# Performance work log

Measured on AMD Instinct MI355X. Metric: run time of the kernel, lower is better.

## Reference

```python
import jax, jax.numpy as jnp
import numpy as np

N_NODES = 50000
N_EDGES = 800000
HIDDEN = 128
N_GRAPHS = 128


def setup_inputs() -> dict:
    key = jax.random.key(0)
    ks = jax.random.split(key, 12)
    x = jax.random.normal(ks[0], (N_NODES, HIDDEN), dtype=jnp.float32)
    edge_index = jax.random.randint(ks[1], (2, N_EDGES), 0, N_NODES, dtype=jnp.int64)
    batch = jnp.sort(jax.random.randint(ks[2], (N_NODES,), 0, N_GRAPHS, dtype=jnp.int64))
    s = 1.0 / np.sqrt(HIDDEN)
    def lin(k):
        return jax.random.uniform(k, (HIDDEN, HIDDEN), jnp.float32, -s, s)
    return {
        "x": x,
        "edge_index": edge_index,
        "batch": batch,
        # layer 1 SAGEConv: lin_l (neighbor, with bias), lin_r (root, no bias)
        "wl1": lin(ks[3]), "b1": jax.random.uniform(ks[4], (HIDDEN,), jnp.float32, -s, s), "wr1": lin(ks[5]),
        # layer 2 SAGEConv
        "wl2": lin(ks[6]), "b2": jax.random.uniform(ks[7], (HIDDEN,), jnp.float32, -s, s), "wr2": lin(ks[8]),
        # classifier Linear
        "cw": lin(ks[9]), "cb": jax.random.uniform(ks[10], (HIDDEN,), jnp.float32, -s, s),
    }


def _sage_conv(x, src, dst, wl, b, wr, n_nodes):
    # mean aggregation of source features onto destination nodes
    agg = jax.ops.segment_sum(x[src], dst, num_segments=n_nodes)      # [N, H]
    deg = jax.ops.segment_sum(jnp.ones_like(dst, x.dtype), dst, num_segments=n_nodes)
    mean = agg / jnp.maximum(deg, 1.0)[:, None]
    # out = lin_l(mean) + lin_r(x); lin_l carries the bias (PyG convention)
    return mean @ wl.T + b + x @ wr.T


def reference(x, edge_index, batch, wl1, b1, wr1, wl2, b2, wr2, cw, cb):
    src, dst = edge_index[0], edge_index[1]
    n = x.shape[0]
    h = jax.nn.relu(_sage_conv(x, src, dst, wl1, b1, wr1, n))
    h = jax.nn.relu(_sage_conv(h, src, dst, wl2, b2, wr2, n))
    # global mean pool over graphs (dropout p=0.0 -> identity)
    gsum = jax.ops.segment_sum(h, batch, num_segments=N_GRAPHS)       # [G, H]
    gcnt = jax.ops.segment_sum(jnp.ones((n,), h.dtype), batch, num_segments=N_GRAPHS)
    pooled = gsum / jnp.maximum(gcnt, 1.0)[:, None]
    return pooled @ cw.T + cb
```

## Files before the change

### kernel.cpp

```cpp
#include <hip/hip_runtime.h>
#include <cstdint>
#include <cstddef>

#define HID 128
#define LDK 72
#define EPB 4096
#define CAP 8192

typedef __attribute__((ext_vector_type(8))) short short8;
typedef __attribute__((ext_vector_type(4))) float floatx4;

#if __has_builtin(__builtin_amdgcn_cvt_pk_f32_fp8) && __has_builtin(__builtin_amdgcn_cvt_pk_fp8_f32)
#define HW_FP8 1
#else
#define HW_FP8 0
#endif

__device__ __forceinline__ unsigned short f2bf(float f) {
  union { float f; uint32_t u; } c; c.f = f;
  uint32_t u = c.u;
  uint32_t r = (u + 0x7FFFu + ((u >> 16) & 1u)) >> 16;
  return (unsigned short)r;
}
__device__ __forceinline__ float bflo(uint32_t v) { return __uint_as_float(v << 16); }
__device__ __forceinline__ float bfhi(uint32_t v) { return __uint_as_float(v & 0xFFFF0000u); }
__device__ __forceinline__ float bf2f(unsigned short s) { return __uint_as_float(((uint32_t)s) << 16); }

__device__ __forceinline__ uint32_t f2fp8_sw(float v) {
  uint32_t u = __float_as_uint(v);
  uint32_t s = (u >> 24) & 0x80u;
  uint32_t af = u & 0x7FFFFFFFu;
  if (__uint_as_float(af) < 0.015625f) return s;
  uint32_t r = af + 0x7FFFFu + ((af >> 20) & 1u);
  return s | ((r >> 20) - 960u);
}
__device__ __forceinline__ float fp8dec_sw(uint32_t b) {
  uint32_t mag = b & 0x7Fu;
  uint32_t v = ((b & 0x80u) << 24) | ((mag << 20) + 0x3C000000u);
  return mag ? __uint_as_float(v) : 0.0f;
}

__device__ __forceinline__ uint32_t pack_fp8x4(float a, float b, float c, float d) {
#if HW_FP8
  int p = __builtin_amdgcn_cvt_pk_fp8_f32(a, b, 0, false);
  p = __builtin_amdgcn_cvt_pk_fp8_f32(c, d, p, true);
  return (uint32_t)p;
#else
  return f2fp8_sw(a) | (f2fp8_sw(b) << 8) | (f2fp8_sw(c) << 16) | (f2fp8_sw(d) << 24);
#endif
}

__device__ __forceinline__ void acc_fp8x4(float* __restrict__ a, uint32_t w) {
#if HW_FP8
  auto lo = __builtin_amdgcn_cvt_pk_f32_fp8(w, false);
  auto hi = __builtin_amdgcn_cvt_pk_f32_fp8(w, true);
  a[0] += lo[0]; a[1] += lo[1]; a[2] += hi[0]; a[3] += hi[1];
#else
  a[0] += fp8dec_sw(w & 255);
  a[1] += fp8dec_sw((w >> 8) & 255);
  a[2] += fp8dec_sw((w >> 16) & 255);
  a[3] += fp8dec_sw(w >> 24);
#endif
}


__global__ __launch_bounds__(256) void k_bucket(const int* __restrict__ src,
                                                const int* __restrict__ dst,
                                                int* __restrict__ bcur,
                                                uint32_t* __restrict__ ebuf,
                                                int E, int NB) {
  __shared__ int hist[256];
  __shared__ int lcur[256];
  const int t = threadIdx.x;
  const int base = blockIdx.x * EPB;
  hist[t] = 0;
  __syncthreads();

  uint32_t val[EPB / 256];
  int bk[EPB / 256];
  #pragma unroll
  for (int i = 0; i < EPB / 256; ++i) {
    int e = base + i * 256 + t;
    bk[i] = -1;
    if (e < E) {
      int d = dst[e];
      int s = src[e];
      bk[i] = d >> 8;
      val[i] = (uint32_t)s | ((uint32_t)(d & 255) << 16);
      atomicAdd(&hist[bk[i]], 1);
    }
  }
  __syncthreads();
  if (t < NB) {
    int c = hist[t];
    lcur[t] = c ? atomicAdd(&bcur[t], c) : 0;
  }
  __syncthreads();
  #pragma unroll
  for (int i = 0; i < EPB / 256; ++i) {
    if (bk[i] >= 0) {
      int pos = bk[i] * CAP + atomicAdd(&lcur[bk[i]], 1);
      ebuf[pos] = val[i];
    }
  }
}

__global__ __launch_bounds__(256) void k_bucket_fill2(const uint32_t* __restrict__ ebuf,
                                                      const int* __restrict__ bcur,
                                                      int* __restrict__ rowbeg,
                                                      int* __restrict__ rowend,
                                                      unsigned short* __restrict__ csr16,
                                                      int N) {
  __shared__ int hist[256];
  __shared__ int scan[256];
  const int b = blockIdx.x;
  const int t = threadIdx.x;
  hist[t] = 0;
  __syncthreads();
  const int lo = b * CAP;
  const int hi = lo + bcur[b];
  for (int i = lo + t; i < hi; i += 256) atomicAdd(&hist[ebuf[i] >> 16], 1);
  __syncthreads();
  int v = hist[t];
  scan[t] = v;
  __syncthreads();
  #pragma unroll
  for (int off = 1; off < 256; off <<= 1) {
    int add = (t >= off) ? scan[t - off] : 0;
    __syncthreads();
    scan[t] += add;
    __syncthreads();
  }
  int excl = scan[t] - v;
  int node = (b << 8) + t;
  if (node < N) {
    rowbeg[node] = lo + excl;
    rowend[node] = lo + excl + v;
  }
  hist[t] = lo + excl;
  __syncthreads();
  for (int i = lo + t; i < hi; i += 256) {
    uint32_t e = ebuf[i];
    int pos = atomicAdd(&hist[e >> 16], 1);
    csr16[pos] = (unsigned short)(e & 0xFFFFu);
  }
}


__global__ __launch_bounds__(256) void k_cast_dual(const float* __restrict__ src,
                                                   unsigned short* __restrict__ dst,
                                                   uint32_t* __restrict__ q, int n4) {
  int i = blockIdx.x * 256 + threadIdx.x;
  if (i < n4) {
    float4 v = ((const float4*)src)[i];
    uint32_t lo = (uint32_t)f2bf(v.x) | ((uint32_t)f2bf(v.y) << 16);
    uint32_t hi = (uint32_t)f2bf(v.z) | ((uint32_t)f2bf(v.w) << 16);
    ((uint2*)dst)[i] = make_uint2(lo, hi);
    q[i] = pack_fp8x4(v.x, v.y, v.z, v.w);
  }
}


__global__ __launch_bounds__(256) void k_cast_bf2q(const unsigned short* __restrict__ src,
                                                   uint32_t* __restrict__ q, int n4) {
  int i = blockIdx.x * 256 + threadIdx.x;
  if (i < n4) {
    uint2 v = ((const uint2*)src)[i];
    q[i] = pack_fp8x4(bflo(v.x), bfhi(v.x), bflo(v.y), bfhi(v.y));
  }
}


__global__ __launch_bounds__(256) void k_aggregate(const unsigned char* __restrict__ featq,
                                                   const int* __restrict__ rowbeg,
                                                   const int* __restrict__ rowend,
                                                   const unsigned short* __restrict__ csr16,
                                                   unsigned short* __restrict__ outmean, int N) {
  int wid = blockIdx.x * 4 + (threadIdx.x >> 6);
  int lane = threadIdx.x & 63;
  if (wid >= N) return;
  int start = rowbeg[wid];
  int end   = rowend[wid];
  const int grp = lane >> 4;
  const int fl  = lane & 15;
  float a[8];
  #pragma unroll
  for (int i = 0; i < 8; ++i) a[i] = 0.f;

  for (int base = start; base < end; base += 64) {
    int m = end - base;
    if (m > 64) m = 64;
    int sidx = (base + lane < end) ? (int)csr16[base + lane] : 0;
    for (int j = 0; j < m; j += 16) {
      int j0 = j + grp, j1 = j + grp + 4, j2 = j + grp + 8, j3 = j + grp + 12;
      int s0 = __shfl(sidx, j0, 64);
      int s1 = __shfl(sidx, j1, 64);
      int s2 = __shfl(sidx, j2, 64);
      int s3 = __shfl(sidx, j3, 64);
      bool g0 = j0 < m, g1 = j1 < m, g2 = j2 < m, g3 = j3 < m;
      uint2 v0, v1, v2, v3;
      if (g0) v0 = *(const uint2*)(featq + (size_t)s0 * HID + fl * 8);
      if (g1) v1 = *(const uint2*)(featq + (size_t)s1 * HID + fl * 8);
      if (g2) v2 = *(const uint2*)(featq + (size_t)s2 * HID + fl * 8);
      if (g3) v3 = *(const uint2*)(featq + (size_t)s3 * HID + fl * 8);
      if (g0) { acc_fp8x4(a, v0.x); acc_fp8x4(a + 4, v0.y); }
      if (g1) { acc_fp8x4(a, v1.x); acc_fp8x4(a + 4, v1.y); }
      if (g2) { acc_fp8x4(a, v2.x); acc_fp8x4(a + 4, v2.y); }
      if (g3) { acc_fp8x4(a, v3.x); acc_fp8x4(a + 4, v3.y); }
    }
  }
  #pragma unroll
  for (int i = 0; i < 8; ++i) {
    a[i] += __shfl_xor(a[i], 16, 64);
    a[i] += __shfl_xor(a[i], 32, 64);
  }
  if (grp == 0) {
    int deg = end - start;
    float inv = 1.0f / (float)(deg > 1 ? deg : 1);
    uint4 o;
    o.x = (uint32_t)f2bf(a[0] * inv) | ((uint32_t)f2bf(a[1] * inv) << 16);
    o.y = (uint32_t)f2bf(a[2] * inv) | ((uint32_t)f2bf(a[3] * inv) << 16);
    o.z = (uint32_t)f2bf(a[4] * inv) | ((uint32_t)f2bf(a[5] * inv) << 16);
    o.w = (uint32_t)f2bf(a[6] * inv) | ((uint32_t)f2bf(a[7] * inv) << 16);
    *(uint4*)(outmean + (size_t)wid * HID + fl * 8) = o;
  }
}


__global__ __launch_bounds__(256, 2) void k_gemm_mfma(const unsigned short* __restrict__ A1,
                                                      const unsigned short* __restrict__ A2,
                                                      const float* __restrict__ WL,
                                                      const float* __restrict__ WR,
                                                      const float* __restrict__ bias,
                                                      unsigned short* __restrict__ outb,
                                                      const int* __restrict__ batch,
                                                      float* __restrict__ pooled,
                                                      int M, int relu) {
  __shared__ __align__(16) unsigned short sAB[2 * 128 * LDK];
  __shared__ int sB[128];
  unsigned short* sA = sAB;
  unsigned short* sW = sAB + 128 * LDK;
  const int t = threadIdx.x;
  const int lane = t & 63;
  const int wave = t >> 6;
  const int row0 = blockIdx.x * 128;
  const int mhalf = (wave & 1) * 64;
  const int nhalf = (wave >> 1) * 64;
  const int ml = lane & 15;
  const int q  = lane >> 4;

  floatx4 acc[4][4];
  #pragma unroll
  for (int a = 0; a < 4; ++a)
    #pragma unroll
    for (int b = 0; b < 4; ++b) acc[a][b] = (floatx4){0.f, 0.f, 0.f, 0.f};

  for (int stage = 0; stage < 4; ++stage) {
    const unsigned short* __restrict__ Asrc = (stage < 2) ? A1 : A2;
    const float* __restrict__ Wsrc = (stage < 2) ? WL : WR;
    const int k0g = (stage & 1) * 64;
    if (stage) __syncthreads();

    #pragma unroll
    for (int i = 0; i < 4; ++i) {
      int seg = t + i * 256;
      int r = seg >> 3, kc = (seg & 7) * 8;
      int gr = row0 + r;
      float4 v = make_float4(0.f, 0.f, 0.f, 0.f);
      if (gr < M) v = *(const float4*)(Asrc + (size_t)gr * HID + k0g + kc);
      *(float4*)&sA[r * LDK + kc] = v;
    }
    #pragma unroll
    for (int i = 0; i < 8; ++i) {
      int e = t + i * 256;
      int o = e >> 4, kc = (e & 15) * 4;
      float4 v = *(const float4*)(Wsrc + (size_t)o * HID + k0g + kc);
      uint32_t lo = (uint32_t)f2bf(v.x) | ((uint32_t)f2bf(v.y) << 16);
      uint32_t hi = (uint32_t)f2bf(v.z) | ((uint32_t)f2bf(v.w) << 16);
      *(uint2*)&sW[o * LDK + kc] = make_uint2(lo, hi);
    }
    __syncthreads();

    #pragma unroll
    for (int ks = 0; ks < 2; ++ks) {
      int kb = ks * 32 + q * 8;
      short8 af[4], bfr[4];
      #pragma unroll
      for (int mt = 0; mt < 4; ++mt)
        af[mt] = *(const short8*)&sA[(mhalf + mt * 16 + ml) * LDK + kb];
      #pragma unroll
      for (int nt = 0; nt < 4; ++nt)
        bfr[nt] = *(const short8*)&sW[(nhalf + nt * 16 + ml) * LDK + kb];
      #pragma unroll
      for (int mt = 0; mt < 4; ++mt)
        #pragma unroll
        for (int nt = 0; nt < 4; ++nt)
          acc[mt][nt] = __builtin_amdgcn_mfma_f32_16x16x32_bf16(af[mt], bfr[nt], acc[mt][nt], 0, 0, 0);
    }
  }

  if (pooled == nullptr) {
    #pragma unroll
    for (int nt = 0; nt < 4; ++nt) {
      int gcol = nhalf + nt * 16 + ml;
      float bv = bias[gcol];
      #pragma unroll
      for (int mt = 0; mt < 4; ++mt) {
        #pragma unroll
        for (int r = 0; r < 4; ++r) {
          int grow = row0 + mhalf + mt * 16 + q * 4 + r;
          if (grow < M) {
            float v = acc[mt][nt][r] + bv;
            if (relu) v = fmaxf(v, 0.f);
            outb[(size_t)grow * HID + gcol] = f2bf(v);
          }
        }
      }
    }
  } else {
    __syncthreads();
    unsigned short* sH = sAB;
    #pragma unroll
    for (int nt = 0; nt < 4; ++nt) {
      int gcol = nhalf + nt * 16 + ml;
      float bv = bias[gcol];
      #pragma unroll
      for (int mt = 0; mt < 4; ++mt) {
        #pragma unroll
        for (int r = 0; r < 4; ++r) {
          int lr = mhalf + mt * 16 + q * 4 + r;
          float v = acc[mt][nt][r] + bv;
          if (relu) v = fmaxf(v, 0.f);
          sH[lr * 128 + gcol] = f2bf(v);
        }
      }
    }
    if (t < 128) sB[t] = (row0 + t < M) ? batch[row0 + t] : -1;
    __syncthreads();
    const int f = t & 127, half = t >> 7;
    float pacc = 0.f;
    int curg = -1;
    for (int n = half; n < 128; n += 2) {
      int g = sB[n];
      if (g != curg) {
        if (curg >= 0) atomicAdd(&pooled[(size_t)curg * HID + f], pacc);
        curg = g; pacc = 0.f;
      }
      if (g >= 0) pacc += bf2f(sH[n * 128 + f]);
    }
    if (curg >= 0) atomicAdd(&pooled[(size_t)curg * HID + f], pacc);
  }
}


__device__ __forceinline__ int lower_bound_dev(const int* a, int n, int key) {
  int lo = 0, hi = n;
  while (lo < hi) {
    int mid = (lo + hi) >> 1;
    if (a[mid] < key) lo = mid + 1; else hi = mid;
  }
  return lo;
}

__global__ __launch_bounds__(256) void k_classify(const float* __restrict__ pooled,
                                                  const int* __restrict__ batch,
                                                  const float* __restrict__ cw,
                                                  const float* __restrict__ cb,
                                                  float* __restrict__ out, int N) {
  __shared__ int bnds[2];
  __shared__ float sp[128];
  __shared__ float part[2][128];
  int g = blockIdx.x;
  int t = threadIdx.x;
  if (t == 0) bnds[0] = lower_bound_dev(batch, N, g);
  if (t == 1) bnds[1] = lower_bound_dev(batch, N, g + 1);
  __syncthreads();
  int cnt = bnds[1] - bnds[0];
  float inv = 1.0f / (float)(cnt > 1 ? cnt : 1);
  if (t < 128) sp[t] = pooled[(size_t)g * HID + t] * inv;
  __syncthreads();
  int o = t & 127, kh = t >> 7;
  float a = 0.f;
  #pragma unroll 4
  for (int k = kh * 64; k < kh * 64 + 64; ++k) a += sp[k] * cw[(size_t)o * HID + k];
  part[kh][o] = a;
  __syncthreads();
  if (t < 128) out[(size_t)g * HID + t] = part[0][t] + part[1][t] + cb[t];
}


extern "C" void kernel_launch(void* const* d_in, const int* in_sizes, int n_in,
                              void* d_out, int out_size, void* d_ws, size_t ws_size,
                              hipStream_t stream) {
  const float* x     = (const float*)d_in[0];
  const int*   ei    = (const int*)d_in[1];
  const int*   batch = (const int*)d_in[2];
  const float* wl1   = (const float*)d_in[3];
  const float* b1    = (const float*)d_in[4];
  const float* wr1   = (const float*)d_in[5];
  const float* wl2   = (const float*)d_in[6];
  const float* b2    = (const float*)d_in[7];
  const float* wr2   = (const float*)d_in[8];
  const float* cw    = (const float*)d_in[9];
  const float* cb    = (const float*)d_in[10];
  float* out = (float*)d_out;

  const int N = in_sizes[0] / HID;
  const int E = in_sizes[1] / 2;
  const int G = out_size / HID;
  const int* src = ei;
  const int* dst = ei + E;

  char* w = (char*)d_ws;
  int*      bcur   = (int*)(w);
  float*    pooled = (float*)(w + 1024);
  int*      rowbeg = (int*)(w + 66560);
  int*      rowend = (int*)(w + 266560);
  uint32_t* ebuf   = (uint32_t*)(w + 466944);
  unsigned short* csr16 = (unsigned short*)(w + 6889472);
  unsigned short* xb    = (unsigned short*)(w + 10100736);
  unsigned short* meanb = (unsigned short*)(w + 10100736 + 12800000);
  unsigned short* h1b   = (unsigned short*)(w + 10100736 + 25600000);
  unsigned char*  xq    = (unsigned char*)(w + 10100736 + 38400000);
  unsigned char*  h1q   = (unsigned char*)(w + 10100736 + 44800000);

  const int NB = (N + 255) >> 8;
  const int aggBlocks  = (N + 3) / 4;
  const int gemmBlocks = (N + 127) / 128;
  const int castBlocks = (N * HID / 4 + 255) / 256;
  const int bktBlocks  = (E + EPB - 1) / EPB;

  hipMemsetAsync(w, 0, 66560, stream);

  hipLaunchKernelGGL(k_bucket,       dim3(bktBlocks), dim3(256), 0, stream, src, dst, bcur, ebuf, E, NB);
  hipLaunchKernelGGL(k_bucket_fill2, dim3(NB),  dim3(256), 0, stream, ebuf, bcur, rowbeg, rowend, csr16, N);
  hipLaunchKernelGGL(k_cast_dual,    dim3(castBlocks), dim3(256), 0, stream, x, xb, (uint32_t*)xq, N * HID / 4);

  hipLaunchKernelGGL(k_aggregate, dim3(aggBlocks), dim3(256), 0, stream, xq, rowbeg, rowend, csr16, meanb, N);
  hipLaunchKernelGGL(k_gemm_mfma, dim3(gemmBlocks), dim3(256), 0, stream, meanb, xb, wl1, wr1, b1, h1b,
                     (const int*)nullptr, (float*)nullptr, N, 1);
  hipLaunchKernelGGL(k_cast_bf2q, dim3(castBlocks), dim3(256), 0, stream, h1b, (uint32_t*)h1q, N * HID / 4);
  hipLaunchKernelGGL(k_aggregate, dim3(aggBlocks), dim3(256), 0, stream, h1q, rowbeg, rowend, csr16, meanb, N);
  hipLaunchKernelGGL(k_gemm_mfma, dim3(gemmBlocks), dim3(256), 0, stream, meanb, h1b, wl2, wr2, b2,
                     (unsigned short*)nullptr, batch, pooled, N, 1);
  hipLaunchKernelGGL(k_classify, dim3(G), dim3(256), 0, stream, pooled, batch, cw, cb, out, N);
}
```

Measured before the change: 229.7 us.

## Fuse fp8 quantization into GEMM epilogue and aggregate two nodes per wave

Removes the separate bf16-to-fp8 cast kernel by writing the fp8 copy of layer-1 output directly from the GEMM epilogue. This saves one launch and one full read and write pass over the hidden features. The aggregation kernel now processes two destination nodes per wavefront, interleaving their gathers to raise memory-level parallelism and halve the wave count. The risks are higher register pressure, imbalance when the two nodes have different degrees, and byte-granular scattered stores in the GEMM epilogue.

Measured after the change: 227.0 us. Within noise of the previous version (-1.2%).

```diff
diff --git a/kernel.cpp b/kernel.cpp
--- a/kernel.cpp
+++ b/kernel.cpp
@@ -47,6 +47,14 @@
   return (uint32_t)p;
 #else
   return f2fp8_sw(a) | (f2fp8_sw(b) << 8) | (f2fp8_sw(c) << 16) | (f2fp8_sw(d) << 24);
+#endif
+}
+
+__device__ __forceinline__ unsigned char f2fp8_one(float v) {
+#if HW_FP8
+  return (unsigned char)(__builtin_amdgcn_cvt_pk_fp8_f32(v, v, 0, false) & 0xFF);
+#else
+  return (unsigned char)f2fp8_sw(v);
 #endif
 }
 
@@ -161,68 +169,87 @@
 }
 
 
-__global__ __launch_bounds__(256) void k_cast_bf2q(const unsigned short* __restrict__ src,
-                                                   uint32_t* __restrict__ q, int n4) {
-  int i = blockIdx.x * 256 + threadIdx.x;
-  if (i < n4) {
-    uint2 v = ((const uint2*)src)[i];
-    q[i] = pack_fp8x4(bflo(v.x), bfhi(v.x), bflo(v.y), bfhi(v.y));
-  }
-}
-
-
 __global__ __launch_bounds__(256) void k_aggregate(const unsigned char* __restrict__ featq,
                                                    const int* __restrict__ rowbeg,
                                                    const int* __restrict__ rowend,
                                                    const unsigned short* __restrict__ csr16,
                                                    unsigned short* __restrict__ outmean, int N) {
-  int wid = blockIdx.x * 4 + (threadIdx.x >> 6);
+  int wpair = blockIdx.x * 4 + (threadIdx.x >> 6);
+  int n0 = wpair * 2;
+  int n1 = n0 + 1;
   int lane = threadIdx.x & 63;
-  if (wid >= N) return;
-  int start = rowbeg[wid];
-  int end   = rowend[wid];
+  if (n0 >= N) return;
   const int grp = lane >> 4;
   const int fl  = lane & 15;
-  float a[8];
-  #pragma unroll
-  for (int i = 0; i < 8; ++i) a[i] = 0.f;
-
-  for (int base = start; base < end; base += 64) {
-    int m = end - base;
-    if (m > 64) m = 64;
-    int sidx = (base + lane < end) ? (int)csr16[base + lane] : 0;
-    for (int j = 0; j < m; j += 16) {
+
+  int b0 = rowbeg[n0], e0 = rowend[n0];
+  int b1 = 0, e1 = 0;
+  if (n1 < N) { b1 = rowbeg[n1]; e1 = rowend[n1]; }
+  const int d0 = e0 - b0, d1 = e1 - b1;
+
+  float a0[8], a1[8];
+  #pragma unroll
+  for (int i = 0; i < 8; ++i) { a0[i] = 0.f; a1[i] = 0.f; }
+
+  while (b0 < e0 || b1 < e1) {
+    int m0 = e0 - b0; if (m0 < 0) m0 = 0; if (m0 > 64) m0 = 64;
+    int m1 = e1 - b1; if (m1 < 0) m1 = 0; if (m1 > 64) m1 = 64;
+    int sidx0 = (b0 + lane < e0) ? (int)csr16[b0 + lane] : 0;
+    int sidx1 = (b1 + lane < e1) ? (int)csr16[b1 + lane] : 0;
+    int mm = m0 > m1 ? m0 : m1;
+    for (int j = 0; j < mm; j += 16) {
       int j0 = j + grp, j1 = j + grp + 4, j2 = j + grp + 8, j3 = j + grp + 12;
-      int s0 = __shfl(sidx, j0, 64);
-      int s1 = __shfl(sidx, j1, 64);
-      int s2 = __shfl(sidx, j2, 64);
-      int s3 = __shfl(sidx, j3, 64);
-      bool g0 = j0 < m, g1 = j1 < m, g2 = j2 < m, g3 = j3 < m;
-      uint2 v0, v1, v2, v3;
-      if (g0) v0 = *(const uint2*)(featq + (size_t)s0 * HID + fl * 8);
-      if (g1) v1 = *(const uint2*)(featq + (size_t)s1 * HID + fl * 8);
-      if (g2) v2 = *(const uint2*)(featq + (size_t)s2 * HID + fl * 8);
-      if (g3) v3 = *(const uint2*)(featq + (size_t)s3 * HID + fl * 8);
-      if (g0) { acc_fp8x4(a, v0.x); acc_fp8x4(a + 4, v0.y); }
-      if (g1) { acc_fp8x4(a, v1.x); acc_fp8x4(a + 4, v1.y); }
-      if (g2) { acc_fp8x4(a, v2.x); acc_fp8x4(a + 4, v2.y); }
-      if (g3) { acc_fp8x4(a, v3.x); acc_fp8x4(a + 4, v3.y); }
-    }
-  }
+      int s00 = __shfl(sidx0, j0, 64), s01 = __shfl(sidx0, j1, 64);
+      int s02 = __shfl(sidx0, j2, 64), s03 = __shfl(sidx0, j3, 64);
+      int s10 = __shfl(sidx1, j0, 64), s11 = __shfl(sidx1, j1, 64);
+      int s12 = __shfl(sidx1, j2, 64), s13 = __shfl(sidx1, j3, 64);
+      bool p00 = j0 < m0, p01 = j1 < m0, p02 = j2 < m0, p03 = j3 < m0;
+      bool p10 = j0 < m1, p11 = j1 < m1, p12 = j2 < m1, p13 = j3 < m1;
+      uint2 u00, u01, u02, u03, u10, u11, u12, u13;
+      if (p00) u00 = *(const uint2*)(featq + (size_t)s00 * HID + fl * 8);
+      if (p01) u01 = *(const uint2*)(featq + (size_t)s01 * HID + fl * 8);
+      if (p02) u02 = *(const uint2*)(featq + (size_t)s02 * HID + fl * 8);
+      if (p03) u03 = *(const uint2*)(featq + (size_t)s03 * HID + fl * 8);
+      if (p10) u10 = *(const uint2*)(featq + (size_t)s10 * HID + fl * 8);
+      if (p11) u11 = *(const uint2*)(featq + (size_t)s11 * HID + fl * 8);
+      if (p12) u12 = *(const uint2*)(featq + (size_t)s12 * HID + fl * 8);
+      if (p13) u13 = *(const uint2*)(featq + (size_t)s13 * HID + fl * 8);
+      if (p00) { acc_fp8x4(a0, u00.x); acc_fp8x4(a0 + 4, u00.y); }
+      if (p01) { acc_fp8x4(a0, u01.x); acc_fp8x4(a0 + 4, u01.y); }
+      if (p02) { acc_fp8x4(a0, u02.x); acc_fp8x4(a0 + 4, u02.y); }
+      if (p03) { acc_fp8x4(a0, u03.x); acc_fp8x4(a0 + 4, u03.y); }
+      if (p10) { acc_fp8x4(a1, u10.x); acc_fp8x4(a1 + 4, u10.y); }
+      if (p11) { acc_fp8x4(a1, u11.x); acc_fp8x4(a1 + 4, u11.y); }
+      if (p12) { acc_fp8x4(a1, u12.x); acc_fp8x4(a1 + 4, u12.y); }
+      if (p13) { acc_fp8x4(a1, u13.x); acc_fp8x4(a1 + 4, u13.y); }
+    }
+    b0 += 64; b1 += 64;
+  }
+
   #pragma unroll
   for (int i = 0; i < 8; ++i) {
-    a[i] += __shfl_xor(a[i], 16, 64);
-    a[i] += __shfl_xor(a[i], 32, 64);
+    a0[i] += __shfl_xor(a0[i], 16, 64);
+    a0[i] += __shfl_xor(a0[i], 32, 64);
+    a1[i] += __shfl_xor(a1[i], 16, 64);
+    a1[i] += __shfl_xor(a1[i], 32, 64);
   }
   if (grp == 0) {
-    int deg = end - start;
-    float inv = 1.0f / (float)(deg > 1 ? deg : 1);
+    float inv0 = 1.0f / (float)(d0 > 1 ? d0 : 1);
     uint4 o;
-    o.x = (uint32_t)f2bf(a[0] * inv) | ((uint32_t)f2bf(a[1] * inv) << 16);
-    o.y = (uint32_t)f2bf(a[2] * inv) | ((uint32_t)f2bf(a[3] * inv) << 16);
-    o.z = (uint32_t)f2bf(a[4] * inv) | ((uint32_t)f2bf(a[5] * inv) << 16);
-    o.w = (uint32_t)f2bf(a[6] * inv) | ((uint32_t)f2bf(a[7] * inv) << 16);
-    *(uint4*)(outmean + (size_t)wid * HID + fl * 8) = o;
+    o.x = (uint32_t)f2bf(a0[0] * inv0) | ((uint32_t)f2bf(a0[1] * inv0) << 16);
+    o.y = (uint32_t)f2bf(a0[2] * inv0) | ((uint32_t)f2bf(a0[3] * inv0) << 16);
+    o.z = (uint32_t)f2bf(a0[4] * inv0) | ((uint32_t)f2bf(a0[5] * inv0) << 16);
+    o.w = (uint32_t)f2bf(a0[6] * inv0) | ((uint32_t)f2bf(a0[7] * inv0) << 16);
+    *(uint4*)(outmean + (size_t)n0 * HID + fl * 8) = o;
+    if (n1 < N) {
+      float inv1 = 1.0f / (float)(d1 > 1 ? d1 : 1);
+      uint4 p;
+      p.x = (uint32_t)f2bf(a1[0] * inv1) | ((uint32_t)f2bf(a1[1] * inv1) << 16);
+      p.y = (uint32_t)f2bf(a1[2] * inv1) | ((uint32_t)f2bf(a1[3] * inv1) << 16);
+      p.z = (uint32_t)f2bf(a1[4] * inv1) | ((uint32_t)f2bf(a1[5] * inv1) << 16);
+      p.w = (uint32_t)f2bf(a1[6] * inv1) | ((uint32_t)f2bf(a1[7] * inv1) << 16);
+      *(uint4*)(outmean + (size_t)n1 * HID + fl * 8) = p;
+    }
   }
 }
 
@@ -233,6 +260,7 @@
                                                       const float* __restrict__ WR,
                                                       const float* __restrict__ bias,
                                                       unsigned short* __restrict__ outb,
+                                                      unsigned char* __restrict__ outq,
                                                       const int* __restrict__ batch,
                                                       float* __restrict__ pooled,
                                                       int M, int relu) {
@@ -313,6 +341,7 @@
             float v = acc[mt][nt][r] + bv;
             if (relu) v = fmaxf(v, 0.f);
             outb[(size_t)grow * HID + gcol] = f2bf(v);
+            if (outq) outq[(size_t)grow * HID + gcol] = f2fp8_one(v);
           }
         }
       }
@@ -425,7 +454,8 @@
   unsigned char*  h1q   = (unsigned char*)(w + 10100736 + 44800000);
 
   const int NB = (N + 255) >> 8;
-  const int aggBlocks  = (N + 3) / 4;
+  const int nPairs = (N + 1) / 2;
+  const int aggBlocks  = (nPairs + 3) / 4;
   const int gemmBlocks = (N + 127) / 128;
   const int castBlocks = (N * HID / 4 + 255) / 256;
   const int bktBlocks  = (E + EPB - 1) / EPB;
@@ -437,11 +467,10 @@
   hipLaunchKernelGGL(k_cast_dual,    dim3(castBlocks), dim3(256), 0, stream, x, xb, (uint32_t*)xq, N * HID / 4);
 
   hipLaunchKernelGGL(k_aggregate, dim3(aggBlocks), dim3(256), 0, stream, xq, rowbeg, rowend, csr16, meanb, N);
-  hipLaunchKernelGGL(k_gemm_mfma, dim3(gemmBlocks), dim3(256), 0, stream, meanb, xb, wl1, wr1, b1, h1b,
+  hipLaunchKernelGGL(k_gemm_mfma, dim3(gemmBlocks), dim3(256), 0, stream, meanb, xb, wl1, wr1, b1, h1b, h1q,
                      (const int*)nullptr, (float*)nullptr, N, 1);
-  hipLaunchKernelGGL(k_cast_bf2q, dim3(castBlocks), dim3(256), 0, stream, h1b, (uint32_t*)h1q, N * HID / 4);
   hipLaunchKernelGGL(k_aggregate, dim3(aggBlocks), dim3(256), 0, stream, h1q, rowbeg, rowend, csr16, meanb, N);
   hipLaunchKernelGGL(k_gemm_mfma, dim3(gemmBlocks), dim3(256), 0, stream, meanb, h1b, wl2, wr2, b2,
-                     (unsigned short*)nullptr, batch, pooled, N, 1);
+                     (unsigned short*)nullptr, (unsigned char*)nullptr, batch, pooled, N, 1);
   hipLaunchKernelGGL(k_classify, dim3(G), dim3(256), 0, stream, pooled, batch, cw, cb, out, N);
 }
```
